# Performance work log

Measured on AMD Instinct MI355X. Metric: run time of the kernel, lower is better.

The kernel has to match this reference:

```python
import jax, jax.numpy as jnp
import numpy as np

ITER = 10
ALPHA = 0.5
SMOOTH = 1.0
EPS = 1e-07


def _maxpool2d(x, win, pad):
    # torch F.max_pool2d pads with -inf for max pooling; reduce_window with -inf init matches exactly
    return jax.lax.reduce_window(
        x, -jnp.inf, jax.lax.max,
        (1, 1, win[0], win[1]), (1, 1, 1, 1),
        [(0, 0), (0, 0), (pad[0], pad[0]), (pad[1], pad[1])])


def soft_erode(x):
    p1 = -_maxpool2d(-x, (3, 1), (1, 0))
    p2 = -_maxpool2d(-x, (1, 3), (0, 1))
    return jnp.minimum(p1, p2)


def soft_dilate(x):
    return _maxpool2d(x, (3, 3), (1, 1))


def soft_open(x):
    return soft_dilate(soft_erode(x))


def soft_skel(img, n_iter):
    skel = jax.nn.relu(img - soft_open(img))

    def body(_, carry):
        im, sk = carry
        im = soft_erode(im)
        delta = jax.nn.relu(im - soft_open(im))
        sk = sk + jax.nn.relu(delta - sk * delta)
        return (im, sk)

    _, skel = jax.lax.fori_loop(0, n_iter, body, (img, skel))
    return skel


def _soft_dice(output, target):
    bs = output.shape[0]
    o = output.reshape(bs, 1, -1)  # binary mode: [B,1,N]
    t = target.reshape(bs, 1, -1)
    inter = jnp.sum(o * t, axis=(0, 2))
    card = jnp.sum(o + t, axis=(0, 2))
    score = (2.0 * inter + SMOOTH) / jnp.maximum(card + SMOOTH, EPS)
    loss = (1.0 - score) * (jnp.sum(t, axis=(0, 2)) > 0).astype(score.dtype)
    return loss.mean()


def _soft_cldice(skel_output, skel_target):
    bs = skel_output.shape[0]
    o = skel_output.reshape(bs, 1, -1)
    t = skel_target.reshape(bs, 1, -1)
    tprec = (jnp.sum(o * t, axis=(0, 2)) + SMOOTH) / (jnp.sum(o, axis=(0, 2)) + SMOOTH)
    tsens = (jnp.sum(t * o, axis=(0, 2)) + SMOOTH) / (jnp.sum(t, axis=(0, 2)) + SMOOTH)
    score = 2.0 * (tprec * tsens) / (tprec + tsens)
    loss = (1.0 - score) * (jnp.sum(t, axis=(0, 2)) > 0).astype(score.dtype)
    return loss.mean()


def setup_inputs() -> dict:
    key = jax.random.key(0)
    k1, k2 = jax.random.split(key)
    output = jax.random.normal(k1, (8, 1, 1024, 1024), dtype=jnp.float32)
    target = jax.random.randint(k2, (8, 1, 1024, 1024), 0, 2).astype(jnp.int32)
    return {"output": output, "target": target}


def reference(output, target):
    # binary mode: logsigmoid(x).exp() == sigmoid(x)
    probs = jax.nn.sigmoid(output)
    tgt = target.astype(probs.dtype)
    dice = _soft_dice(probs, tgt)
    skel_o = soft_skel(probs, ITER)
    skel_t = soft_skel(tgt, ITER)
    cl_dice = _soft_cldice(skel_o, skel_t)
    return (1.0 - ALPHA) * dice + ALPHA * cl_dice
```

## Files before the change

### kernel.cpp

```cpp
#include <hip/hip_runtime.h>
#include <math.h>


#define HH 1024
#define WW 1024
#define BATCH 8
#define HW (HH * WW)
#define NITER 10
#define TW 128
#define TH 64
#define AH 88
#define CXC 20
#define NCELL (AH * CXC)
#define BMP 6
#define NQO 440
#define NT 1024
#define NBX 8
#define NBY 16
#define NBLK (NBX * NBY * BATCH)

typedef _Float16 h8 __attribute__((ext_vector_type(8)));
typedef unsigned int u32;
typedef unsigned long long u64;
typedef u32 u4v __attribute__((ext_vector_type(4)));

#define MIN2(a, b) __builtin_elementwise_min(a, b)
#define MAX2(a, b) __builtin_elementwise_max(a, b)

__device__ __forceinline__ u32 alignb(u32 hi, u32 lo) {
    return (u32)((((u64)hi << 32) | lo) >> 16);
}
__device__ __forceinline__ u32 fsh(u32 hi, u32 lo, int s) {
    return (u32)((((u64)hi << 32) | lo) >> s);
}
__device__ __forceinline__ u32 dw0(h8 v) { return __builtin_bit_cast(u4v, v).x; }
__device__ __forceinline__ u32 dw3(h8 v) { return __builtin_bit_cast(u4v, v).w; }
__device__ __forceinline__ h8 shl1(h8 v, u32 l3) {
    u4v d = __builtin_bit_cast(u4v, v);
    u4v r;
    r.x = alignb(d.x, l3); r.y = alignb(d.y, d.x);
    r.z = alignb(d.z, d.y); r.w = alignb(d.w, d.z);
    return __builtin_bit_cast(h8, r);
}
__device__ __forceinline__ h8 shr1(h8 v, u32 r0d) {
    u4v d = __builtin_bit_cast(u4v, v);
    u4v r;
    r.x = alignb(d.y, d.x); r.y = alignb(d.z, d.y);
    r.z = alignb(d.w, d.z); r.w = alignb(r0d, d.w);
    return __builtin_bit_cast(h8, r);
}
__device__ __forceinline__ float sigm(float x) { return 1.0f / (1.0f + __expf(-x)); }
__device__ __forceinline__ int imin(int a, int b) { return a < b ? a : b; }
__device__ __forceinline__ int imax(int a, int b) { return a > b ? a : b; }

__global__ __launch_bounds__(NT) void cldice_mega_kernel(const float* __restrict__ logits,
                                                         const int* __restrict__ target,
                                                         float* __restrict__ partials) {
    __shared__ __align__(16) h8 bufO[NCELL];
    __shared__ u32 bmT[AH * BMP];
    __shared__ u32 pub[256];
    __shared__ float red[96];

    const int tid = threadIdx.x;
    const int img = blockIdx.z;
    const int x0 = blockIdx.x * TW, y0 = blockIdx.y * TH;

    const _Float16 HIF = (_Float16)__builtin_inff();
    const h8 HI8 = (h8)HIF;
    const h8 LO8 = (h8)(-HIF);
    const h8 Z8 = (h8)(_Float16)0;

    const bool has_e = tid < NQO;
    int e_base = CXC, e_M = 0;
    bool e_rok[4] = {false, false, false, false};
    if (has_e) {
        int q = tid / 20, c = tid - (tid / 20) * 20;
        int r = 1 + 4 * q;
        if (r > 83) r = 83;
        e_base = r * CXC + c;
        int cMx = imin(8 * c + 7, 159 - 8 * c);
#pragma unroll
        for (int k = 0; k < 4; ++k)
            e_M = imax(e_M, imin(imin(r + k, 87 - (r + k)), cMx));
        bool colOOB = (x0 == 0 && c < 2) || (x0 == WW - TW && c >= 18);
#pragma unroll
        for (int k = 0; k < 4; ++k)
            e_rok[k] = !colOOB && ((unsigned)(y0 - 12 + r + k) < HH);
    }

    const bool has_o = (tid >= 512) && (tid < 768);
    const int op = tid & 255;
    const int opr = op >> 4, oc = op & 15;
    const int orow = 12 + 4 * opr;
    const int ob = orow * CXC + 2 + oc;
    const bool rT = (y0 == 0 && opr == 0);
    const bool rB = (y0 == HH - TH && opr == 15);
    const bool cL = (x0 == 0 && oc == 0);
    const bool cR = (x0 == WW - TW && oc == 15);

    const bool has_te = (tid >= 768) && (tid < 768 + 22 * BMP);
    int tb = BMP, te_M = 0;
    u32 oobm = 0;
    bool trok[4] = {false, false, false, false};
    if (has_te) {
        int p = tid - 768;
        int q = p / BMP, c = p - (p / BMP) * BMP;
        int r = 1 + 4 * q;
        if (r > 83) r = 83;
        tb = r * BMP + c;
        int pxlo = imax(32 * c - 16, 0), pxhi = imin(32 * c + 15, 159);
        int cMx = imin(pxhi, 159 - pxlo);
#pragma unroll
        for (int k = 0; k < 4; ++k)
            te_M = imax(te_M, imin(imin(r + k, 87 - (r + k)), cMx));
        if (c == 0) oobm |= 0x0000FFFFu;
        if (c == 5) oobm |= 0xFFFF0000u;
        if (x0 == 0 && c == 0) oobm = 0xFFFFFFFFu;
        if (x0 == WW - TW && c == 5) oobm = 0xFFFFFFFFu;
#pragma unroll
        for (int k = 0; k < 4; ++k)
            trok[k] = (unsigned)(y0 - 12 + r + k) < HH;
    }

    const bool has_to = tid >= 960;
    const int tp = tid - 960;
    const int topr = (tp >> 2) & 15, td = (tp & 3) + 1;
    const int torow = 12 + 4 * topr;
    const int tob = torow * BMP + td;
    const bool trT = (y0 == 0 && topr == 0);
    const bool trB = (y0 == HH - TH && topr == 15);
    const bool tcL = (x0 == 0 && td == 1);
    const bool tcR = (x0 == WW - TW && td == 4);

    if (tid < AH) {
        unsigned short* p16 = (unsigned short*)bmT;
        p16[tid * 12 + 0] = 0xFFFFu;
        p16[tid * 12 + 11] = 0xFFFFu;
    }

    float d_inter = 0.f, d_card = 0.f, d_st = 0.f;
#pragma unroll
    for (int s = 0; s < 2; ++s) {
        int li = tid + NT * s;
        if (li < NCELL) {
            int r = li / CXC, c = li - (li / CXC) * CXC;
            int gy = y0 - 12 + r, gx = x0 - 16 + 8 * c;
            bool gyok = (unsigned)gy < HH;
            float vo[8];
            u32 tb8 = 0;
            if (gyok && gx >= 0 && gx + 7 < WW) {
                int g = img * HW + gy * WW + gx;
                float4 a = *(const float4*)(logits + g);
                float4 b = *(const float4*)(logits + g + 4);
                vo[0] = sigm(a.x); vo[1] = sigm(a.y); vo[2] = sigm(a.z); vo[3] = sigm(a.w);
                vo[4] = sigm(b.x); vo[5] = sigm(b.y); vo[6] = sigm(b.z); vo[7] = sigm(b.w);
                int4 p = *(const int4*)(target + g);
                int4 q = *(const int4*)(target + g + 4);
                tb8 = (p.x != 0 ? 1u : 0u) | (p.y != 0 ? 2u : 0u) |
                      (p.z != 0 ? 4u : 0u) | (p.w != 0 ? 8u : 0u) |
                      (q.x != 0 ? 16u : 0u) | (q.y != 0 ? 32u : 0u) |
                      (q.z != 0 ? 64u : 0u) | (q.w != 0 ? 128u : 0u);
            } else {
#pragma unroll
                for (int j = 0; j < 8; ++j) {
                    int gxx = gx + j;
                    if (gyok && (unsigned)gxx < WW) {
                        int g = img * HW + gy * WW + gxx;
                        vo[j] = sigm(logits[g]);
                        tb8 |= (target[g] != 0 ? 1u : 0u) << j;
                    } else { vo[j] = INFINITY; tb8 |= 1u << j; }
                }
            }
            h8 ho;
#pragma unroll
            for (int j = 0; j < 8; ++j) ho[j] = (_Float16)vo[j];
            bufO[li] = ho;
            ((unsigned char*)bmT)[r * 24 + 2 + c] = (unsigned char)tb8;
            if (r >= 12 && r < 76 && c >= 2 && c < 18) {
#pragma unroll
                for (int j = 0; j < 8; ++j) {
                    float t = (float)((tb8 >> j) & 1u);
                    d_inter += t * vo[j];
                    d_card += vo[j] + t;
                    d_st += t;
                }
            }
        }
    }
    __syncthreads();
    h8 imv[4], sk[4];
    if (has_o) {
#pragma unroll
        for (int k = 0; k < 4; ++k) imv[k] = bufO[ob + k * CXC];
    }
#pragma unroll
    for (int k = 0; k < 4; ++k) sk[k] = Z8;
    u32 timv[4] = {0, 0, 0, 0}, tsk[4] = {0, 0, 0, 0};
    if (has_to) {
#pragma unroll
        for (int k = 0; k < 4; ++k) timv[k] = bmT[tob + k * BMP];
    }

    for (int L = 1; L <= NITER + 1; ++L) {
        h8 eo[4];
        const bool act = has_e && (L <= e_M);
        if (act) {
            const h8* b = bufO;
            h8 u  = b[e_base - CXC];
            h8 c0 = b[e_base],           c1 = b[e_base + CXC];
            h8 c2 = b[e_base + 2 * CXC], c3 = b[e_base + 3 * CXC];
            h8 d  = b[e_base + 4 * CXC];
            h8 l0 = b[e_base - 1],           l1 = b[e_base + CXC - 1];
            h8 l2 = b[e_base + 2 * CXC - 1], l3 = b[e_base + 3 * CXC - 1];
            h8 r0 = b[e_base + 1],           r1 = b[e_base + CXC + 1];
            h8 r2 = b[e_base + 2 * CXC + 1], r3 = b[e_base + 3 * CXC + 1];
            h8 p01 = MIN2(c0, c1), p12 = MIN2(c1, c2), p23 = MIN2(c2, c3);
            h8 v0 = MIN2(u, p01), v1 = MIN2(p01, c2), v2 = MIN2(p12, c3), v3 = MIN2(p23, d);
            eo[0] = MIN2(v0, MIN2(shl1(c0, dw3(l0)), shr1(c0, dw0(r0))));
            eo[1] = MIN2(v1, MIN2(shl1(c1, dw3(l1)), shr1(c1, dw0(r1))));
            eo[2] = MIN2(v2, MIN2(shl1(c2, dw3(l2)), shr1(c2, dw0(r2))));
            eo[3] = MIN2(v3, MIN2(shl1(c3, dw3(l3)), shr1(c3, dw0(r3))));
        }
        u32 et[4];
        const bool actt = has_te && (L <= te_M);
        if (actt) {
            u32 m0 = bmT[tb - BMP], m1 = bmT[tb], m2 = bmT[tb + BMP];
            u32 m3 = bmT[tb + 2 * BMP], m4 = bmT[tb + 3 * BMP], m5 = bmT[tb + 4 * BMP];
            u32 lw0 = bmT[tb - 1],           lw1 = bmT[tb + BMP - 1];
            u32 lw2 = bmT[tb + 2 * BMP - 1], lw3 = bmT[tb + 3 * BMP - 1];
            u32 rw0 = bmT[tb + 1],           rw1 = bmT[tb + BMP + 1];
            u32 rw2 = bmT[tb + 2 * BMP + 1], rw3 = bmT[tb + 3 * BMP + 1];
            u32 p12 = m1 & m2, p23 = m2 & m3, p34 = m3 & m4;
            u32 v0 = m0 & p12, v1 = p12 & m3, v2 = p23 & m4, v3 = p34 & m5;
            et[0] = v0 & fsh(m1, lw0, 31) & fsh(rw0, m1, 1);
            et[1] = v1 & fsh(m2, lw1, 31) & fsh(rw1, m2, 1);
            et[2] = v2 & fsh(m3, lw2, 31) & fsh(rw2, m3, 1);
            et[3] = v3 & fsh(m4, lw3, 31) & fsh(rw3, m4, 1);
        }
        __syncthreads();
        if (act) {
#pragma unroll
            for (int k = 0; k < 4; ++k)
                bufO[e_base + k * CXC] = e_rok[k] ? eo[k] : HI8;
        }
        if (actt) {
#pragma unroll
            for (int k = 0; k < 4; ++k)
                bmT[tb + k * BMP] = trok[k] ? (et[k] | oobm) : 0xFFFFFFFFu;
        }
        __syncthreads();
        if (has_o) {
            h8 m0 = bufO[ob - CXC], m1 = bufO[ob], m2 = bufO[ob + CXC];
            h8 m3 = bufO[ob + 2 * CXC], m4 = bufO[ob + 3 * CXC], m5 = bufO[ob + 4 * CXC];
            h8 nm0 = m1, nm1 = m2, nm2 = m3, nm3 = m4;
            if (rT) m0 = LO8;
            if (rB) m5 = LO8;
            h8 q12 = MAX2(m1, m2), q34 = MAX2(m3, m4);
            h8 Mc0 = MAX2(m0, q12), Mc1 = MAX2(q12, m3);
            h8 Mc2 = MAX2(m2, q34), Mc3 = MAX2(q34, m5);
            h8 a0 = bufO[ob - CXC - 1], a1 = bufO[ob - 1], a2 = bufO[ob + CXC - 1];
            h8 a3 = bufO[ob + 2 * CXC - 1], a4 = bufO[ob + 3 * CXC - 1], a5 = bufO[ob + 4 * CXC - 1];
            if (rT) a0 = LO8;
            if (rB) a5 = LO8;
            h8 s12 = MAX2(a1, a2), s34 = MAX2(a3, a4);
            h8 Ml0 = MAX2(a0, s12), Ml1 = MAX2(s12, a3);
            h8 Ml2 = MAX2(a2, s34), Ml3 = MAX2(s34, a5);
            if (cL) { Ml0 = LO8; Ml1 = LO8; Ml2 = LO8; Ml3 = LO8; }
            h8 b0 = bufO[ob - CXC + 1], b1 = bufO[ob + 1], b2 = bufO[ob + CXC + 1];
            h8 b3 = bufO[ob + 2 * CXC + 1], b4 = bufO[ob + 3 * CXC + 1], b5 = bufO[ob + 4 * CXC + 1];
            if (rT) b0 = LO8;
            if (rB) b5 = LO8;
            h8 t12 = MAX2(b1, b2), t34 = MAX2(b3, b4);
            h8 Mr0 = MAX2(b0, t12), Mr1 = MAX2(t12, b3);
            h8 Mr2 = MAX2(b2, t34), Mr3 = MAX2(t34, b5);
            if (cR) { Mr0 = LO8; Mr1 = LO8; Mr2 = LO8; Mr3 = LO8; }
            h8 o0 = MAX2(Mc0, MAX2(shl1(Mc0, dw3(Ml0)), shr1(Mc0, dw0(Mr0))));
            h8 o1 = MAX2(Mc1, MAX2(shl1(Mc1, dw3(Ml1)), shr1(Mc1, dw0(Mr1))));
            h8 o2 = MAX2(Mc2, MAX2(shl1(Mc2, dw3(Ml2)), shr1(Mc2, dw0(Mr2))));
            h8 o3 = MAX2(Mc3, MAX2(shl1(Mc3, dw3(Ml3)), shr1(Mc3, dw0(Mr3))));
            h8 d0 = MAX2(imv[0] - o0, Z8);
            h8 d1 = MAX2(imv[1] - o1, Z8);
            h8 d2 = MAX2(imv[2] - o2, Z8);
            h8 d3 = MAX2(imv[3] - o3, Z8);
            if (L == 1) { sk[0] = d0; sk[1] = d1; sk[2] = d2; sk[3] = d3; }
            else {
                sk[0] = sk[0] + MAX2(d0 - sk[0] * d0, Z8);
                sk[1] = sk[1] + MAX2(d1 - sk[1] * d1, Z8);
                sk[2] = sk[2] + MAX2(d2 - sk[2] * d2, Z8);
                sk[3] = sk[3] + MAX2(d3 - sk[3] * d3, Z8);
            }
            imv[0] = nm0; imv[1] = nm1; imv[2] = nm2; imv[3] = nm3;
        }
        if (has_to) {
            u32 m0 = bmT[tob - BMP], m1 = bmT[tob], m2 = bmT[tob + BMP];
            u32 m3 = bmT[tob + 2 * BMP], m4 = bmT[tob + 3 * BMP], m5 = bmT[tob + 4 * BMP];
            u32 nm0 = m1, nm1 = m2, nm2 = m3, nm3 = m4;
            u32 l0 = bmT[tob - BMP - 1], l1 = bmT[tob - 1], l2 = bmT[tob + BMP - 1];
            u32 l3 = bmT[tob + 2 * BMP - 1], l4 = bmT[tob + 3 * BMP - 1], l5 = bmT[tob + 4 * BMP - 1];
            u32 r0 = bmT[tob - BMP + 1], r1 = bmT[tob + 1], r2 = bmT[tob + BMP + 1];
            u32 r3 = bmT[tob + 2 * BMP + 1], r4 = bmT[tob + 3 * BMP + 1], r5 = bmT[tob + 4 * BMP + 1];
            if (trT) { m0 = 0; l0 = 0; r0 = 0; }
            if (trB) { m5 = 0; l5 = 0; r5 = 0; }
            if (tcL) { l0 = 0; l1 = 0; l2 = 0; l3 = 0; l4 = 0; l5 = 0; }
            if (tcR) { r0 = 0; r1 = 0; r2 = 0; r3 = 0; r4 = 0; r5 = 0; }
            u32 q12 = m1 | m2, q34 = m3 | m4;
            u32 Vc0 = m0 | q12, Vc1 = q12 | m3, Vc2 = m2 | q34, Vc3 = q34 | m5;
            u32 s12 = l1 | l2, s34 = l3 | l4;
            u32 Vl0 = l0 | s12, Vl1 = s12 | l3, Vl2 = l2 | s34, Vl3 = s34 | l5;
            u32 t12 = r1 | r2, t34 = r3 | r4;
            u32 Vr0 = r0 | t12, Vr1 = t12 | r3, Vr2 = r2 | t34, Vr3 = t34 | r5;
            u32 o0 = Vc0 | fsh(Vc0, Vl0, 31) | fsh(Vr0, Vc0, 1);
            u32 o1 = Vc1 | fsh(Vc1, Vl1, 31) | fsh(Vr1, Vc1, 1);
            u32 o2 = Vc2 | fsh(Vc2, Vl2, 31) | fsh(Vr2, Vc2, 1);
            u32 o3 = Vc3 | fsh(Vc3, Vl3, 31) | fsh(Vr3, Vc3, 1);
            tsk[0] |= timv[0] & ~o0;
            tsk[1] |= timv[1] & ~o1;
            tsk[2] |= timv[2] & ~o2;
            tsk[3] |= timv[3] & ~o3;
            timv[0] = nm0; timv[1] = nm1; timv[2] = nm2; timv[3] = nm3;
        }
    }

    __syncthreads();
    float I = 0.f, So = 0.f, St = 0.f;
    if (has_to) {
#pragma unroll
        for (int k = 0; k < 4; ++k) {
            pub[(tp << 2) + k] = tsk[k];
            St += (float)__popc(tsk[k]);
        }
    }
    __syncthreads();
    if (has_o) {
        int tt = (opr << 2) + (oc >> 2);
        int sh = (oc & 3) * 8;
#pragma unroll
        for (int k = 0; k < 4; ++k) {
            u32 w = pub[(tt << 2) + k] >> sh;
#pragma unroll
            for (int j = 0; j < 8; ++j) {
                float a = (float)sk[k][j];
                So += a;
                if ((w >> j) & 1u) I += a;
            }
        }
    }

    float v6[6] = {d_inter, d_card, d_st, I, So, St};
#pragma unroll
    for (int q = 0; q < 6; ++q)
        for (int off = 32; off > 0; off >>= 1) v6[q] += __shfl_down(v6[q], off);
    int lane = tid & 63, w = tid >> 6;
    if (lane == 0) {
#pragma unroll
        for (int q = 0; q < 6; ++q) red[w * 6 + q] = v6[q];
    }
    __syncthreads();
    if (tid == 0) {
        int bid = (blockIdx.z * gridDim.y + blockIdx.y) * gridDim.x + blockIdx.x;
#pragma unroll
        for (int q = 0; q < 6; ++q) {
            float s = 0.f;
#pragma unroll
            for (int ww = 0; ww < 16; ++ww) s += red[ww * 6 + q];
            partials[q * NBLK + bid] = s;
        }
    }
}

__global__ __launch_bounds__(1024) void final_kernel(const float* __restrict__ partials,
                                                     float* __restrict__ out) {
    float s[6] = {0.f, 0.f, 0.f, 0.f, 0.f, 0.f};
    for (int i = threadIdx.x; i < NBLK; i += 1024) {
#pragma unroll
        for (int q = 0; q < 6; ++q) s[q] += partials[q * NBLK + i];
    }
#pragma unroll
    for (int q = 0; q < 6; ++q)
        for (int off = 32; off > 0; off >>= 1) s[q] += __shfl_down(s[q], off);
    __shared__ float red[96];
    int lane = threadIdx.x & 63, w = threadIdx.x >> 6;
    if (lane == 0) {
#pragma unroll
        for (int q = 0; q < 6; ++q) red[w * 6 + q] = s[q];
    }
    __syncthreads();
    if (threadIdx.x == 0) {
        float t[6];
#pragma unroll
        for (int q = 0; q < 6; ++q) {
            float a = 0.f;
#pragma unroll
            for (int ww = 0; ww < 16; ++ww) a += red[ww * 6 + q];
            t[q] = a;
        }
        float inter = t[0], card = t[1], sumt = t[2];
        float I = t[3], So = t[4], St = t[5];
        float score_d = (2.0f * inter + 1.0f) / fmaxf(card + 1.0f, 1e-7f);
        float dice = (1.0f - score_d) * (sumt > 0.0f ? 1.0f : 0.0f);
        float tprec = (I + 1.0f) / (So + 1.0f);
        float tsens = (I + 1.0f) / (St + 1.0f);
        float score_c = 2.0f * (tprec * tsens) / (tprec + tsens);
        float cl = (1.0f - score_c) * (St > 0.0f ? 1.0f : 0.0f);
        out[0] = 0.5f * dice + 0.5f * cl;
    }
}

extern "C" void kernel_launch(void* const* d_in, const int* in_sizes, int n_in,
                              void* d_out, int out_size, void* d_ws, size_t ws_size,
                              hipStream_t stream) {
    const float* logits = (const float*)d_in[0];
    const int* target = (const int*)d_in[1];
    float* out = (float*)d_out;
    float* partials = (float*)d_ws;

    dim3 grid(NBX, NBY, BATCH);
    cldice_mega_kernel<<<grid, NT, 0, stream>>>(logits, target, partials);
    final_kernel<<<1, 1024, 0, stream>>>(partials, out);
}
```

Before: 181.2 us.

## Double-buffer shared tiles to halve barriers per erosion iteration

Ping-pong buffers for the float16 image and the target bitmask in shared memory. Each phase now reads one buffer and writes the other, and the opening step for iteration L runs one phase late, after the erode for L+1. This leaves one __syncthreads per phase instead of two, and it lets the erode and open work groups run in the same phase. The cost is double the shared memory for bufO and bmT, which may reduce occupancy. The erode counts are also capped at NITER+1.

Result: faster. 169.6 us, median of 2 (-6.4%).

```diff
diff --git a/kernel.cpp b/kernel.cpp
--- a/kernel.cpp
+++ b/kernel.cpp
@@ -56,8 +56,8 @@
 __global__ __launch_bounds__(NT) void cldice_mega_kernel(const float* __restrict__ logits,
                                                          const int* __restrict__ target,
                                                          float* __restrict__ partials) {
-    __shared__ __align__(16) h8 bufO[NCELL];
-    __shared__ u32 bmT[AH * BMP];
+    __shared__ __align__(16) h8 bufO[2][NCELL];
+    __shared__ u32 bmT[2][AH * BMP];
     __shared__ u32 pub[256];
     __shared__ float red[96];
 
@@ -82,6 +82,7 @@
 #pragma unroll
         for (int k = 0; k < 4; ++k)
             e_M = imax(e_M, imin(imin(r + k, 87 - (r + k)), cMx));
+        e_M = imin(e_M, NITER + 1);
         bool colOOB = (x0 == 0 && c < 2) || (x0 == WW - TW && c >= 18);
 #pragma unroll
         for (int k = 0; k < 4; ++k)
@@ -113,6 +114,7 @@
 #pragma unroll
         for (int k = 0; k < 4; ++k)
             te_M = imax(te_M, imin(imin(r + k, 87 - (r + k)), cMx));
+        te_M = imin(te_M, NITER + 1);
         if (c == 0) oobm |= 0x0000FFFFu;
         if (c == 5) oobm |= 0xFFFF0000u;
         if (x0 == 0 && c == 0) oobm = 0xFFFFFFFFu;
@@ -133,9 +135,12 @@
     const bool tcR = (x0 == WW - TW && td == 4);
 
     if (tid < AH) {
-        unsigned short* p16 = (unsigned short*)bmT;
+        unsigned short* p16 = (unsigned short*)bmT[0];
         p16[tid * 12 + 0] = 0xFFFFu;
         p16[tid * 12 + 11] = 0xFFFFu;
+        unsigned short* q16 = (unsigned short*)bmT[1];
+        q16[tid * 12 + 0] = 0xFFFFu;
+        q16[tid * 12 + 11] = 0xFFFFu;
     }
 
     float d_inter = 0.f, d_card = 0.f, d_st = 0.f;
@@ -174,8 +179,8 @@
             h8 ho;
 #pragma unroll
             for (int j = 0; j < 8; ++j) ho[j] = (_Float16)vo[j];
-            bufO[li] = ho;
-            ((unsigned char*)bmT)[r * 24 + 2 + c] = (unsigned char)tb8;
+            bufO[0][li] = ho;
+            ((unsigned char*)bmT[0])[r * 24 + 2 + c] = (unsigned char)tb8;
             if (r >= 12 && r < 76 && c >= 2 && c < 18) {
 #pragma unroll
                 for (int j = 0; j < 8; ++j) {
@@ -191,137 +196,150 @@
     h8 imv[4], sk[4];
     if (has_o) {
 #pragma unroll
-        for (int k = 0; k < 4; ++k) imv[k] = bufO[ob + k * CXC];
+        for (int k = 0; k < 4; ++k) imv[k] = bufO[0][ob + k * CXC];
     }
 #pragma unroll
     for (int k = 0; k < 4; ++k) sk[k] = Z8;
     u32 timv[4] = {0, 0, 0, 0}, tsk[4] = {0, 0, 0, 0};
     if (has_to) {
 #pragma unroll
-        for (int k = 0; k < 4; ++k) timv[k] = bmT[tob + k * BMP];
-    }
-
-    for (int L = 1; L <= NITER + 1; ++L) {
-        h8 eo[4];
-        const bool act = has_e && (L <= e_M);
-        if (act) {
-            const h8* b = bufO;
-            h8 u  = b[e_base - CXC];
-            h8 c0 = b[e_base],           c1 = b[e_base + CXC];
-            h8 c2 = b[e_base + 2 * CXC], c3 = b[e_base + 3 * CXC];
-            h8 d  = b[e_base + 4 * CXC];
-            h8 l0 = b[e_base - 1],           l1 = b[e_base + CXC - 1];
-            h8 l2 = b[e_base + 2 * CXC - 1], l3 = b[e_base + 3 * CXC - 1];
-            h8 r0 = b[e_base + 1],           r1 = b[e_base + CXC + 1];
-            h8 r2 = b[e_base + 2 * CXC + 1], r3 = b[e_base + 3 * CXC + 1];
-            h8 p01 = MIN2(c0, c1), p12 = MIN2(c1, c2), p23 = MIN2(c2, c3);
-            h8 v0 = MIN2(u, p01), v1 = MIN2(p01, c2), v2 = MIN2(p12, c3), v3 = MIN2(p23, d);
-            eo[0] = MIN2(v0, MIN2(shl1(c0, dw3(l0)), shr1(c0, dw0(r0))));
-            eo[1] = MIN2(v1, MIN2(shl1(c1, dw3(l1)), shr1(c1, dw0(r1))));
-            eo[2] = MIN2(v2, MIN2(shl1(c2, dw3(l2)), shr1(c2, dw0(r2))));
-            eo[3] = MIN2(v3, MIN2(shl1(c3, dw3(l3)), shr1(c3, dw0(r3))));
-        }
-        u32 et[4];
-        const bool actt = has_te && (L <= te_M);
-        if (actt) {
-            u32 m0 = bmT[tb - BMP], m1 = bmT[tb], m2 = bmT[tb + BMP];
-            u32 m3 = bmT[tb + 2 * BMP], m4 = bmT[tb + 3 * BMP], m5 = bmT[tb + 4 * BMP];
-            u32 lw0 = bmT[tb - 1],           lw1 = bmT[tb + BMP - 1];
-            u32 lw2 = bmT[tb + 2 * BMP - 1], lw3 = bmT[tb + 3 * BMP - 1];
-            u32 rw0 = bmT[tb + 1],           rw1 = bmT[tb + BMP + 1];
-            u32 rw2 = bmT[tb + 2 * BMP + 1], rw3 = bmT[tb + 3 * BMP + 1];
-            u32 p12 = m1 & m2, p23 = m2 & m3, p34 = m3 & m4;
-            u32 v0 = m0 & p12, v1 = p12 & m3, v2 = p23 & m4, v3 = p34 & m5;
-            et[0] = v0 & fsh(m1, lw0, 31) & fsh(rw0, m1, 1);
-            et[1] = v1 & fsh(m2, lw1, 31) & fsh(rw1, m2, 1);
-            et[2] = v2 & fsh(m3, lw2, 31) & fsh(rw2, m3, 1);
-            et[3] = v3 & fsh(m4, lw3, 31) & fsh(rw3, m4, 1);
-        }
-        __syncthreads();
-        if (act) {
-#pragma unroll
-            for (int k = 0; k < 4; ++k)
-                bufO[e_base + k * CXC] = e_rok[k] ? eo[k] : HI8;
-        }
-        if (actt) {
-#pragma unroll
-            for (int k = 0; k < 4; ++k)
-                bmT[tb + k * BMP] = trok[k] ? (et[k] | oobm) : 0xFFFFFFFFu;
-        }
-        __syncthreads();
-        if (has_o) {
-            h8 m0 = bufO[ob - CXC], m1 = bufO[ob], m2 = bufO[ob + CXC];
-            h8 m3 = bufO[ob + 2 * CXC], m4 = bufO[ob + 3 * CXC], m5 = bufO[ob + 4 * CXC];
-            h8 nm0 = m1, nm1 = m2, nm2 = m3, nm3 = m4;
-            if (rT) m0 = LO8;
-            if (rB) m5 = LO8;
-            h8 q12 = MAX2(m1, m2), q34 = MAX2(m3, m4);
-            h8 Mc0 = MAX2(m0, q12), Mc1 = MAX2(q12, m3);
-            h8 Mc2 = MAX2(m2, q34), Mc3 = MAX2(q34, m5);
-            h8 a0 = bufO[ob - CXC - 1], a1 = bufO[ob - 1], a2 = bufO[ob + CXC - 1];
-            h8 a3 = bufO[ob + 2 * CXC - 1], a4 = bufO[ob + 3 * CXC - 1], a5 = bufO[ob + 4 * CXC - 1];
-            if (rT) a0 = LO8;
-            if (rB) a5 = LO8;
-            h8 s12 = MAX2(a1, a2), s34 = MAX2(a3, a4);
-            h8 Ml0 = MAX2(a0, s12), Ml1 = MAX2(s12, a3);
-            h8 Ml2 = MAX2(a2, s34), Ml3 = MAX2(s34, a5);
-            if (cL) { Ml0 = LO8; Ml1 = LO8; Ml2 = LO8; Ml3 = LO8; }
-            h8 b0 = bufO[ob - CXC + 1], b1 = bufO[ob + 1], b2 = bufO[ob + CXC + 1];
-            h8 b3 = bufO[ob + 2 * CXC + 1], b4 = bufO[ob + 3 * CXC + 1], b5 = bufO[ob + 4 * CXC + 1];
-            if (rT) b0 = LO8;
-            if (rB) b5 = LO8;
-            h8 t12 = MAX2(b1, b2), t34 = MAX2(b3, b4);
-            h8 Mr0 = MAX2(b0, t12), Mr1 = MAX2(t12, b3);
-            h8 Mr2 = MAX2(b2, t34), Mr3 = MAX2(t34, b5);
-            if (cR) { Mr0 = LO8; Mr1 = LO8; Mr2 = LO8; Mr3 = LO8; }
-            h8 o0 = MAX2(Mc0, MAX2(shl1(Mc0, dw3(Ml0)), shr1(Mc0, dw0(Mr0))));
-            h8 o1 = MAX2(Mc1, MAX2(shl1(Mc1, dw3(Ml1)), shr1(Mc1, dw0(Mr1))));
-            h8 o2 = MAX2(Mc2, MAX2(shl1(Mc2, dw3(Ml2)), shr1(Mc2, dw0(Mr2))));
-            h8 o3 = MAX2(Mc3, MAX2(shl1(Mc3, dw3(Ml3)), shr1(Mc3, dw0(Mr3))));
-            h8 d0 = MAX2(imv[0] - o0, Z8);
-            h8 d1 = MAX2(imv[1] - o1, Z8);
-            h8 d2 = MAX2(imv[2] - o2, Z8);
-            h8 d3 = MAX2(imv[3] - o3, Z8);
-            if (L == 1) { sk[0] = d0; sk[1] = d1; sk[2] = d2; sk[3] = d3; }
-            else {
-                sk[0] = sk[0] + MAX2(d0 - sk[0] * d0, Z8);
-                sk[1] = sk[1] + MAX2(d1 - sk[1] * d1, Z8);
-                sk[2] = sk[2] + MAX2(d2 - sk[2] * d2, Z8);
-                sk[3] = sk[3] + MAX2(d3 - sk[3] * d3, Z8);
-            }
-            imv[0] = nm0; imv[1] = nm1; imv[2] = nm2; imv[3] = nm3;
-        }
-        if (has_to) {
-            u32 m0 = bmT[tob - BMP], m1 = bmT[tob], m2 = bmT[tob + BMP];
-            u32 m3 = bmT[tob + 2 * BMP], m4 = bmT[tob + 3 * BMP], m5 = bmT[tob + 4 * BMP];
-            u32 nm0 = m1, nm1 = m2, nm2 = m3, nm3 = m4;
-            u32 l0 = bmT[tob - BMP - 1], l1 = bmT[tob - 1], l2 = bmT[tob + BMP - 1];
-            u32 l3 = bmT[tob + 2 * BMP - 1], l4 = bmT[tob + 3 * BMP - 1], l5 = bmT[tob + 4 * BMP - 1];
-            u32 r0 = bmT[tob - BMP + 1], r1 = bmT[tob + 1], r2 = bmT[tob + BMP + 1];
-            u32 r3 = bmT[tob + 2 * BMP + 1], r4 = bmT[tob + 3 * BMP + 1], r5 = bmT[tob + 4 * BMP + 1];
-            if (trT) { m0 = 0; l0 = 0; r0 = 0; }
-            if (trB) { m5 = 0; l5 = 0; r5 = 0; }
-            if (tcL) { l0 = 0; l1 = 0; l2 = 0; l3 = 0; l4 = 0; l5 = 0; }
-            if (tcR) { r0 = 0; r1 = 0; r2 = 0; r3 = 0; r4 = 0; r5 = 0; }
-            u32 q12 = m1 | m2, q34 = m3 | m4;
-            u32 Vc0 = m0 | q12, Vc1 = q12 | m3, Vc2 = m2 | q34, Vc3 = q34 | m5;
-            u32 s12 = l1 | l2, s34 = l3 | l4;
-            u32 Vl0 = l0 | s12, Vl1 = s12 | l3, Vl2 = l2 | s34, Vl3 = s34 | l5;
-            u32 t12 = r1 | r2, t34 = r3 | r4;
-            u32 Vr0 = r0 | t12, Vr1 = t12 | r3, Vr2 = r2 | t34, Vr3 = t34 | r5;
-            u32 o0 = Vc0 | fsh(Vc0, Vl0, 31) | fsh(Vr0, Vc0, 1);
-            u32 o1 = Vc1 | fsh(Vc1, Vl1, 31) | fsh(Vr1, Vc1, 1);
-            u32 o2 = Vc2 | fsh(Vc2, Vl2, 31) | fsh(Vr2, Vc2, 1);
-            u32 o3 = Vc3 | fsh(Vc3, Vl3, 31) | fsh(Vr3, Vc3, 1);
-            tsk[0] |= timv[0] & ~o0;
-            tsk[1] |= timv[1] & ~o1;
-            tsk[2] |= timv[2] & ~o2;
-            tsk[3] |= timv[3] & ~o3;
-            timv[0] = nm0; timv[1] = nm1; timv[2] = nm2; timv[3] = nm3;
-        }
-    }
-
-    __syncthreads();
+        for (int k = 0; k < 4; ++k) timv[k] = bmT[0][tob + k * BMP];
+    }
+
+#define PHASE(LV, rdO, wrO, rdT, wrT)                                              \
+    {                                                                              \
+        const int PL = (LV);                                                       \
+                           \
+        if (has_e && PL <= e_M) {                                                  \
+            const h8* b = (rdO);                                                   \
+            h8 u  = b[e_base - CXC];                                               \
+            h8 c0 = b[e_base],           c1 = b[e_base + CXC];                     \
+            h8 c2 = b[e_base + 2 * CXC], c3 = b[e_base + 3 * CXC];                 \
+            h8 d  = b[e_base + 4 * CXC];                                           \
+            h8 l0 = b[e_base - 1],           l1 = b[e_base + CXC - 1];             \
+            h8 l2 = b[e_base + 2 * CXC - 1], l3 = b[e_base + 3 * CXC - 1];         \
+            h8 r0 = b[e_base + 1],           r1 = b[e_base + CXC + 1];             \
+            h8 r2 = b[e_base + 2 * CXC + 1], r3 = b[e_base + 3 * CXC + 1];         \
+            h8 p01 = MIN2(c0, c1), p12 = MIN2(c1, c2), p23 = MIN2(c2, c3);         \
+            h8 v0 = MIN2(u, p01), v1 = MIN2(p01, c2);                              \
+            h8 v2 = MIN2(p12, c3), v3 = MIN2(p23, d);                              \
+            h8 eo0 = MIN2(v0, MIN2(shl1(c0, dw3(l0)), shr1(c0, dw0(r0))));         \
+            h8 eo1 = MIN2(v1, MIN2(shl1(c1, dw3(l1)), shr1(c1, dw0(r1))));         \
+            h8 eo2 = MIN2(v2, MIN2(shl1(c2, dw3(l2)), shr1(c2, dw0(r2))));         \
+            h8 eo3 = MIN2(v3, MIN2(shl1(c3, dw3(l3)), shr1(c3, dw0(r3))));         \
+            (wrO)[e_base]           = e_rok[0] ? eo0 : HI8;                        \
+            (wrO)[e_base + CXC]     = e_rok[1] ? eo1 : HI8;                        \
+            (wrO)[e_base + 2 * CXC] = e_rok[2] ? eo2 : HI8;                        \
+            (wrO)[e_base + 3 * CXC] = e_rok[3] ? eo3 : HI8;                        \
+        }                                                                          \
+                                              \
+        if (has_te && PL <= te_M) {                                                \
+            const u32* bt = (rdT);                                                 \
+            u32 m0 = bt[tb - BMP], m1 = bt[tb], m2 = bt[tb + BMP];                 \
+            u32 m3 = bt[tb + 2 * BMP], m4 = bt[tb + 3 * BMP], m5 = bt[tb + 4 * BMP]; \
+            u32 lw0 = bt[tb - 1],           lw1 = bt[tb + BMP - 1];                \
+            u32 lw2 = bt[tb + 2 * BMP - 1], lw3 = bt[tb + 3 * BMP - 1];            \
+            u32 rw0 = bt[tb + 1],           rw1 = bt[tb + BMP + 1];                \
+            u32 rw2 = bt[tb + 2 * BMP + 1], rw3 = bt[tb + 3 * BMP + 1];            \
+            u32 p12 = m1 & m2, p23 = m2 & m3, p34 = m3 & m4;                       \
+            u32 v0 = m0 & p12, v1 = p12 & m3, v2 = p23 & m4, v3 = p34 & m5;        \
+            u32 et0 = v0 & fsh(m1, lw0, 31) & fsh(rw0, m1, 1);                     \
+            u32 et1 = v1 & fsh(m2, lw1, 31) & fsh(rw1, m2, 1);                     \
+            u32 et2 = v2 & fsh(m3, lw2, 31) & fsh(rw2, m3, 1);                     \
+            u32 et3 = v3 & fsh(m4, lw3, 31) & fsh(rw3, m4, 1);                     \
+            (wrT)[tb]           = trok[0] ? (et0 | oobm) : 0xFFFFFFFFu;            \
+            (wrT)[tb + BMP]     = trok[1] ? (et1 | oobm) : 0xFFFFFFFFu;            \
+            (wrT)[tb + 2 * BMP] = trok[2] ? (et2 | oobm) : 0xFFFFFFFFu;            \
+            (wrT)[tb + 3 * BMP] = trok[3] ? (et3 | oobm) : 0xFFFFFFFFu;            \
+        }                                                                          \
+                \
+        if (has_o && PL >= 2) {                                                    \
+            const h8* b = (rdO);                                                   \
+            h8 m0 = b[ob - CXC], m1 = b[ob], m2 = b[ob + CXC];                     \
+            h8 m3 = b[ob + 2 * CXC], m4 = b[ob + 3 * CXC], m5 = b[ob + 4 * CXC];  \
+            h8 nm0 = m1, nm1 = m2, nm2 = m3, nm3 = m4;                             \
+            if (rT) m0 = LO8;                                                      \
+            if (rB) m5 = LO8;                                                      \
+            h8 q12 = MAX2(m1, m2), q34 = MAX2(m3, m4);                             \
+            h8 Mc0 = MAX2(m0, q12), Mc1 = MAX2(q12, m3);                           \
+            h8 Mc2 = MAX2(m2, q34), Mc3 = MAX2(q34, m5);                           \
+            h8 a0 = b[ob - CXC - 1], a1 = b[ob - 1], a2 = b[ob + CXC - 1];         \
+            h8 a3 = b[ob + 2 * CXC - 1], a4 = b[ob + 3 * CXC - 1];                 \
+            h8 a5 = b[ob + 4 * CXC - 1];                                           \
+            if (rT) a0 = LO8;                                                      \
+            if (rB) a5 = LO8;                                                      \
+            h8 s12 = MAX2(a1, a2), s34 = MAX2(a3, a4);                             \
+            h8 Ml0 = MAX2(a0, s12), Ml1 = MAX2(s12, a3);                           \
+            h8 Ml2 = MAX2(a2, s34), Ml3 = MAX2(s34, a5);                           \
+            if (cL) { Ml0 = LO8; Ml1 = LO8; Ml2 = LO8; Ml3 = LO8; }                \
+            h8 b0 = b[ob - CXC + 1], b1 = b[ob + 1], b2 = b[ob + CXC + 1];         \
+            h8 b3 = b[ob + 2 * CXC + 1], b4 = b[ob + 3 * CXC + 1];                 \
+            h8 b5 = b[ob + 4 * CXC + 1];                                           \
+            if (rT) b0 = LO8;                                                      \
+            if (rB) b5 = LO8;                                                      \
+            h8 t12 = MAX2(b1, b2), t34 = MAX2(b3, b4);                             \
+            h8 Mr0 = MAX2(b0, t12), Mr1 = MAX2(t12, b3);                           \
+            h8 Mr2 = MAX2(b2, t34), Mr3 = MAX2(t34, b5);                           \
+            if (cR) { Mr0 = LO8; Mr1 = LO8; Mr2 = LO8; Mr3 = LO8; }                \
+            h8 o0 = MAX2(Mc0, MAX2(shl1(Mc0, dw3(Ml0)), shr1(Mc0, dw0(Mr0))));     \
+            h8 o1 = MAX2(Mc1, MAX2(shl1(Mc1, dw3(Ml1)), shr1(Mc1, dw0(Mr1))));     \
+            h8 o2 = MAX2(Mc2, MAX2(shl1(Mc2, dw3(Ml2)), shr1(Mc2, dw0(Mr2))));     \
+            h8 o3 = MAX2(Mc3, MAX2(shl1(Mc3, dw3(Ml3)), shr1(Mc3, dw0(Mr3))));     \
+            h8 d0 = MAX2(imv[0] - o0, Z8);                                         \
+            h8 d1 = MAX2(imv[1] - o1, Z8);                                         \
+            h8 d2 = MAX2(imv[2] - o2, Z8);                                         \
+            h8 d3 = MAX2(imv[3] - o3, Z8);                                         \
+            if (PL == 2) { sk[0] = d0; sk[1] = d1; sk[2] = d2; sk[3] = d3; }       \
+            else {                                                                 \
+                sk[0] = sk[0] + MAX2(d0 - sk[0] * d0, Z8);                         \
+                sk[1] = sk[1] + MAX2(d1 - sk[1] * d1, Z8);                         \
+                sk[2] = sk[2] + MAX2(d2 - sk[2] * d2, Z8);                         \
+                sk[3] = sk[3] + MAX2(d3 - sk[3] * d3, Z8);                         \
+            }                                                                      \
+            imv[0] = nm0; imv[1] = nm1; imv[2] = nm2; imv[3] = nm3;                \
+        }                                                                          \
+                            \
+        if (has_to && PL >= 2) {                                                   \
+            const u32* bt = (rdT);                                                 \
+            u32 m0 = bt[tob - BMP], m1 = bt[tob], m2 = bt[tob + BMP];              \
+            u32 m3 = bt[tob + 2 * BMP], m4 = bt[tob + 3 * BMP];                    \
+            u32 m5 = bt[tob + 4 * BMP];                                            \
+            u32 nm0 = m1, nm1 = m2, nm2 = m3, nm3 = m4;                            \
+            u32 l0 = bt[tob - BMP - 1], l1 = bt[tob - 1], l2 = bt[tob + BMP - 1];  \
+            u32 l3 = bt[tob + 2 * BMP - 1], l4 = bt[tob + 3 * BMP - 1];            \
+            u32 l5 = bt[tob + 4 * BMP - 1];                                        \
+            u32 r0 = bt[tob - BMP + 1], r1 = bt[tob + 1], r2 = bt[tob + BMP + 1];  \
+            u32 r3 = bt[tob + 2 * BMP + 1], r4 = bt[tob + 3 * BMP + 1];            \
+            u32 r5 = bt[tob + 4 * BMP + 1];                                        \
+            if (trT) { m0 = 0; l0 = 0; r0 = 0; }                                   \
+            if (trB) { m5 = 0; l5 = 0; r5 = 0; }                                   \
+            if (tcL) { l0 = 0; l1 = 0; l2 = 0; l3 = 0; l4 = 0; l5 = 0; }           \
+            if (tcR) { r0 = 0; r1 = 0; r2 = 0; r3 = 0; r4 = 0; r5 = 0; }           \
+            u32 q12 = m1 | m2, q34 = m3 | m4;                                      \
+            u32 Vc0 = m0 | q12, Vc1 = q12 | m3, Vc2 = m2 | q34, Vc3 = q34 | m5;    \
+            u32 s12 = l1 | l2, s34 = l3 | l4;                                      \
+            u32 Vl0 = l0 | s12, Vl1 = s12 | l3, Vl2 = l2 | s34, Vl3 = s34 | l5;    \
+            u32 t12 = r1 | r2, t34 = r3 | r4;                                      \
+            u32 Vr0 = r0 | t12, Vr1 = t12 | r3, Vr2 = r2 | t34, Vr3 = t34 | r5;    \
+            u32 o0 = Vc0 | fsh(Vc0, Vl0, 31) | fsh(Vr0, Vc0, 1);                   \
+            u32 o1 = Vc1 | fsh(Vc1, Vl1, 31) | fsh(Vr1, Vc1, 1);                   \
+            u32 o2 = Vc2 | fsh(Vc2, Vl2, 31) | fsh(Vr2, Vc2, 1);                   \
+            u32 o3 = Vc3 | fsh(Vc3, Vl3, 31) | fsh(Vr3, Vc3, 1);                   \
+            tsk[0] |= timv[0] & ~o0;                                               \
+            tsk[1] |= timv[1] & ~o1;                                               \
+            tsk[2] |= timv[2] & ~o2;                                               \
+            tsk[3] |= timv[3] & ~o3;                                               \
+            timv[0] = nm0; timv[1] = nm1; timv[2] = nm2; timv[3] = nm3;            \
+        }                                                                          \
+        __syncthreads();                                                           \
+    }
+
+    for (int L = 1; L <= NITER + 2; L += 2) {
+        PHASE(L,     bufO[0], bufO[1], bmT[0], bmT[1])
+        PHASE(L + 1, bufO[1], bufO[0], bmT[1], bmT[0])
+    }
+#undef PHASE
+
     float I = 0.f, So = 0.f, St = 0.f;
     if (has_to) {
 #pragma unroll
```
